# Performance work log

Hardware: AMD Instinct MI355X
Metric: run time of the kernel (lower is better)

The kernel has to match this reference:

```python
import jax, jax.numpy as jnp
import numpy as np

N, E, B = 50000, 800000, 16
IN_DIM, ED, HD, SD, NC = 64, 8, 128, 128, 8
T_STEPS = (8 + 16) // 2  # eval mode: (t_min + t_max) // 2 = 12


def setup_inputs() -> dict:
    key = jax.random.key(0)
    ks = jax.random.split(key, 12)
    s = 0.05  # small init scale so 12 residual steps stay bounded
    return {
        "x": jax.random.normal(ks[0], (N, IN_DIM), jnp.float32),
        "edge_index": jax.random.randint(ks[1], (2, E), 0, N, jnp.int64),
        "edge_attr": jax.random.normal(ks[2], (E, ED), jnp.float32),
        "batch": jnp.sort(jax.random.randint(ks[3], (N,), 0, B, jnp.int64)),
        "enc_w": jax.random.normal(ks[4], (IN_DIM, SD), jnp.float32) * s,
        "enc_b": jnp.zeros((SD,), jnp.float32),
        "msg_w": jax.random.normal(ks[5], (SD + ED, HD), jnp.float32) * s,
        "msg_b": jnp.zeros((HD,), jnp.float32),
        "up_w1": jax.random.normal(ks[6], (SD + HD, HD), jnp.float32) * s,
        "up_b1": jnp.zeros((HD,), jnp.float32),
        "up_w2": jax.random.normal(ks[7], (HD, SD), jnp.float32) * s,
        "up_b2": jnp.zeros((SD,), jnp.float32),
    }


def reference(x, edge_index, edge_attr, batch, enc_w, enc_b, msg_w, msg_b,
              up_w1, up_b1, up_w2, up_b2):
    src, dst = edge_index[0], edge_index[1]  # x_j = x[src], aggregate at dst
    # in-degree for mean aggregation (zero-degree nodes get 0, clamp avoids /0)
    deg = jax.ops.segment_sum(jnp.ones((E,), x.dtype), dst, num_segments=N)
    deg = jnp.clip(deg, 1.0)[:, None]

    # Encoder: Linear + ReLU
    state = jax.nn.relu(x @ enc_w + enc_b)  # [N, SD]

    for _ in range(T_STEPS):
        # message: relu(W_msg @ [h_j || e_ji])
        m = jax.nn.relu(jnp.concatenate([state[src], edge_attr], axis=-1) @ msg_w + msg_b)  # [E, HD]
        agg = jax.ops.segment_sum(m, dst, num_segments=N) / deg  # scatter-mean [N, HD]
        # update MLP on [h_i || m_bar_i]
        h = jax.nn.relu(jnp.concatenate([state, agg], axis=-1) @ up_w1 + up_b1)
        delta = h @ up_w2 + up_b2
        state = state + delta  # eval: no stochastic mask, no noise

    # Readout: per-graph mean over class channels
    class_ch = state[:, -NC:]  # [N, NC]
    cnt = jax.ops.segment_sum(jnp.ones((N,), x.dtype), batch, num_segments=B)
    logits = jax.ops.segment_sum(class_ch, batch, num_segments=B) / jnp.clip(cnt, 1.0)[:, None]
    return logits
```

## Files before the change

### kernel.cpp

```cpp
#include <hip/hip_runtime.h>
#include <hip/hip_bf16.h>

#define NN 50000
#define NE 800000
#define NB 16
#define T_STEPS 12
#define SCAN_B 196
#define EAW_BLOCKS 1024

typedef __attribute__((ext_vector_type(8))) short short8;
typedef __attribute__((ext_vector_type(4))) float f32x4;
typedef __attribute__((ext_vector_type(2))) float f32x2;
typedef unsigned short u16;
typedef unsigned int u32;

__device__ __forceinline__ float bf2f(u32 u) {
    union { u32 i; float f; } v; v.i = u << 16; return v.f;
}
__device__ __forceinline__ u16 f2bf(float f) {
    union { float f; u32 i; } v; v.f = f;
    u32 r = v.i + 0x7fffu + ((v.i >> 16) & 1u);
    return (u16)(r >> 16);
}
__device__ __forceinline__ f32x4 mfma16(short8 a, short8 b, f32x4 c) {
    return __builtin_amdgcn_mfma_f32_16x16x32_bf16(a, b, c, 0, 0, 0);
}

__device__ __forceinline__ u32 pk2_fp8(float o0, float o1) {
#if __has_builtin(__builtin_amdgcn_cvt_pk_fp8_f32)
    return (u32)__builtin_amdgcn_cvt_pk_fp8_f32(o0, o1, 0, false);
#else
    u32 a = 0;
    asm("v_cvt_pk_fp8_f32 %0, %1, %2" : "+v"(a) : "v"(o0), "v"(o1));
    return a;
#endif
}
__device__ __forceinline__ u32 pk4_fp8(float o0, float o1, float o2, float o3) {
    return (pk2_fp8(o0, o1) & 0xffffu) | (pk2_fp8(o2, o3) << 16);
}

__device__ __forceinline__ void fp8x4f(u32 w, float& f0, float& f1, float& f2, float& f3) {
#if __has_builtin(__builtin_amdgcn_cvt_pk_f32_fp8)
    f32x2 r0 = __builtin_amdgcn_cvt_pk_f32_fp8((int)w, false);
    f32x2 r1 = __builtin_amdgcn_cvt_pk_f32_fp8((int)w, true);
    f0 = r0[0]; f1 = r0[1]; f2 = r1[0]; f3 = r1[1];
#else
    f32x2 r0, r1;
    u32 hi = w >> 16;
    asm("v_cvt_pk_f32_fp8 %0, %1" : "=v"(r0) : "v"(w));
    asm("v_cvt_pk_f32_fp8 %0, %1" : "=v"(r1) : "v"(hi));
    f0 = r0[0]; f1 = r0[1]; f2 = r1[0]; f3 = r1[1];
#endif
}

#define W1OFF 0
#define W2OFF 32768
#define WSOFF 49152
#define ENCOFF 65536
#define PACKN 73728


__global__ void k_hist(const int* __restrict__ dst, int* __restrict__ hist) {
    int e = blockIdx.x * 256 + threadIdx.x;
    if (e < NE) atomicAdd(&hist[dst[e]], 1);
}

__global__ void k_scanA(const int* __restrict__ hist, int* __restrict__ excl,
                        int* __restrict__ bsum) {
    __shared__ int sh[256];
    int t = threadIdx.x, b = blockIdx.x;
    int idx = b * 256 + t;
    int v = (idx < NN) ? hist[idx] : 0;
    sh[t] = v;
    __syncthreads();
    for (int off = 1; off < 256; off <<= 1) {
        int add = (t >= off) ? sh[t - off] : 0;
        __syncthreads();
        sh[t] += add;
        __syncthreads();
    }
    if (idx < NN) excl[idx] = sh[t] - v;
    if (t == 255) bsum[b] = sh[255];
}

__global__ void k_scanB(int* __restrict__ bsum) {
    __shared__ int sh[256];
    int t = threadIdx.x;
    int v = (t < SCAN_B) ? bsum[t] : 0;
    sh[t] = v;
    __syncthreads();
    for (int off = 1; off < 256; off <<= 1) {
        int add = (t >= off) ? sh[t - off] : 0;
        __syncthreads();
        sh[t] += add;
        __syncthreads();
    }
    if (t < SCAN_B) bsum[t] = sh[t] - v;
}

__global__ void k_scanC(const int* __restrict__ excl, const int* __restrict__ bsum,
                        int* __restrict__ rowptr, int* __restrict__ cursor) {
    int idx = blockIdx.x * 256 + threadIdx.x;
    if (idx < NN) {
        int r = excl[idx] + bsum[blockIdx.x];
        rowptr[idx] = r;
        cursor[idx] = r;
    }
    if (idx == 0) rowptr[NN] = NE;
}

__global__ void k_scatter(const int* __restrict__ src, const int* __restrict__ dst,
                          const float* __restrict__ eattr, int* __restrict__ cursor,
                          int* __restrict__ ssrc, u16* __restrict__ ea8) {
    int e = blockIdx.x * 256 + threadIdx.x;
    if (e >= NE) return;
    int d = dst[e];
    int pos = atomicAdd(&cursor[d], 1);
    ssrc[pos] = src[e];
    const float* ap = eattr + (size_t)e * 8;
    uint4 w;
    w.x = (u32)f2bf(ap[0]) | ((u32)f2bf(ap[1]) << 16);
    w.y = (u32)f2bf(ap[2]) | ((u32)f2bf(ap[3]) << 16);
    w.z = (u32)f2bf(ap[4]) | ((u32)f2bf(ap[5]) << 16);
    w.w = (u32)f2bf(ap[6]) | ((u32)f2bf(ap[7]) << 16);
    *(uint4*)(ea8 + (size_t)pos * 8) = w;
}

__global__ __launch_bounds__(256) void k_eaw(
    const u16* __restrict__ ea8, const float* __restrict__ msg_w,
    unsigned char* __restrict__ eaw) {
    const int tid = threadIdx.x;
    const int oct = tid & 7;
    const int esub = tid >> 3;
    float w[8][16];
#pragma unroll
    for (int k = 0; k < 8; ++k) {
#pragma unroll
        for (int c4 = 0; c4 < 4; ++c4) {
            float4 v = *(const float4*)(msg_w + (size_t)(128 + k) * 128 + oct * 16 + c4 * 4);
            w[k][c4 * 4 + 0] = v.x; w[k][c4 * 4 + 1] = v.y;
            w[k][c4 * 4 + 2] = v.z; w[k][c4 * 4 + 3] = v.w;
        }
    }
    int e = blockIdx.x * 32 + esub;
    if (e >= NE) return;
    uint4 ev = *(const uint4*)(ea8 + (size_t)e * 8);
    while (true) {
        int en = e + EAW_BLOCKS * 32;
        bool more = en < NE;
        uint4 evn;
        if (more) evn = *(const uint4*)(ea8 + (size_t)en * 8);
        float ef[8];
        ef[0] = bf2f(ev.x & 0xffffu); ef[1] = bf2f(ev.x >> 16);
        ef[2] = bf2f(ev.y & 0xffffu); ef[3] = bf2f(ev.y >> 16);
        ef[4] = bf2f(ev.z & 0xffffu); ef[5] = bf2f(ev.z >> 16);
        ef[6] = bf2f(ev.w & 0xffffu); ef[7] = bf2f(ev.w >> 16);
        float o[16];
#pragma unroll
        for (int c = 0; c < 16; ++c) o[c] = ef[0] * w[0][c];
#pragma unroll
        for (int k = 1; k < 8; ++k)
#pragma unroll
            for (int c = 0; c < 16; ++c) o[c] += ef[k] * w[k][c];
        uint4 q;
        q.x = pk4_fp8(o[0], o[1], o[2], o[3]);
        q.y = pk4_fp8(o[4], o[5], o[6], o[7]);
        q.z = pk4_fp8(o[8], o[9], o[10], o[11]);
        q.w = pk4_fp8(o[12], o[13], o[14], o[15]);
        *(uint4*)(eaw + (size_t)e * 128 + oct * 16) = q;
        if (!more) break;
        ev = evn;
        e = en;
    }
}

__global__ void k_pack(const float* __restrict__ up_w1, const float* __restrict__ up_w2,
                       const float* __restrict__ msg_w, const float* __restrict__ enc_w,
                       u16* __restrict__ packed) {
    int idx = blockIdx.x * 256 + threadIdx.x;
    if (idx >= PACKN) return;
    const float* srcp; int local;
    if (idx < W2OFF)        { srcp = up_w1; local = idx; }
    else if (idx < WSOFF)   { srcp = up_w2; local = idx - W2OFF; }
    else if (idx < ENCOFF)  { srcp = msg_w; local = idx - WSOFF; }
    else                    { srcp = enc_w; local = idx - ENCOFF; }
    int j = local & 7;
    int l = (local >> 3) & 63;
    int ntks = local >> 9;
    int nt = ntks & 7;
    int ks = ntks >> 3;
    int krow = ks * 32 + (l >> 4) * 8 + j;
    int col = nt * 16 + (l & 15);
    packed[idx] = f2bf(srcp[krow * 128 + col]);
}


__global__ __launch_bounds__(256) void k_encode(
    const float* __restrict__ x, const float* __restrict__ enc_b,
    const float* __restrict__ msg_b, const u16* __restrict__ packed,
    float* __restrict__ state_f, u16* __restrict__ state_h, u16* __restrict__ swb) {
    __shared__ u16 stage[4][2048];
    const int wv = threadIdx.x >> 6, l = threadIdx.x & 63;
    const int lr = l & 15, kb = l >> 4;
    const int rb = blockIdx.x * 64 + wv * 16;
    const int row = rb + lr;
    const int rowc = row < NN ? row : NN - 1;

    f32x4 acc[8] = {};
#pragma unroll
    for (int ks = 0; ks < 2; ++ks) {
        const float* ap = x + (size_t)rowc * 64 + ks * 32 + kb * 8;
        float4 a0 = *(const float4*)ap;
        float4 a1 = *(const float4*)(ap + 4);
        short8 a;
        a[0] = (short)f2bf(a0.x); a[1] = (short)f2bf(a0.y);
        a[2] = (short)f2bf(a0.z); a[3] = (short)f2bf(a0.w);
        a[4] = (short)f2bf(a1.x); a[5] = (short)f2bf(a1.y);
        a[6] = (short)f2bf(a1.z); a[7] = (short)f2bf(a1.w);
        const u16* bp = packed + ENCOFF + (size_t)(ks * 512 + l) * 8;
#pragma unroll
        for (int nt = 0; nt < 8; ++nt) {
            short8 b = *(const short8*)(bp + nt * 512);
            acc[nt] = mfma16(a, b, acc[nt]);
        }
    }
#pragma unroll
    for (int nt = 0; nt < 8; ++nt) {
        int col = nt * 16 + lr;
        float bias = enc_b[col];
#pragma unroll
        for (int j = 0; j < 4; ++j) {
            int rl = kb * 4 + j;
            int r = rb + rl;
            float v = acc[nt][j] + bias;
            v = v > 0.f ? v : 0.f;
            u16 h = f2bf(v);
            if (r < NN) {
                state_f[(size_t)r * 128 + col] = v;
                state_h[(size_t)r * 128 + col] = h;
            }
            int byte = (rl * 256 + col * 2) ^ ((rl & 7) << 4);
            *(u16*)((char*)stage[wv] + byte) = h;
        }
    }
    f32x4 acc3[8] = {};
#pragma unroll
    for (int ks = 0; ks < 4; ++ks) {
        int byte = (lr * 256 + ks * 64 + kb * 16) ^ ((lr & 7) << 4);
        short8 a = *(const short8*)((char*)stage[wv] + byte);
        const u16* bp = packed + WSOFF + (size_t)(ks * 512 + l) * 8;
#pragma unroll
        for (int nt = 0; nt < 8; ++nt) {
            short8 b = *(const short8*)(bp + nt * 512);
            acc3[nt] = mfma16(a, b, acc3[nt]);
        }
    }
#pragma unroll
    for (int nt = 0; nt < 8; ++nt) {
        int col = nt * 16 + lr;
        float bias = msg_b[col];
#pragma unroll
        for (int j = 0; j < 4; ++j) {
            int r = rb + kb * 4 + j;
            if (r < NN) swb[(size_t)r * 128 + col] = f2bf(acc3[nt][j] + bias);
        }
    }
}


__global__ __launch_bounds__(256) void k_edge(
    const int* __restrict__ rowptr, const int* __restrict__ ssrc,
    const unsigned char* __restrict__ eaw, const u16* __restrict__ swb,
    u16* __restrict__ aggb) {
    const int wv = threadIdx.x >> 6, l = threadIdx.x & 63;
    const int half = l >> 5, lo = l & 31;
    const int n = blockIdx.x * 8 + wv * 2 + half;
    if (n >= NN) return;
    const int e0 = rowptr[n], e1 = rowptr[n + 1];
    const unsigned char* ep = eaw + (size_t)e0 * 128 + 4 * lo;
    const u16* swbase = swb + 4 * lo;
    float a0 = 0.f, a1 = 0.f, a2 = 0.f, a3 = 0.f;
#pragma unroll 4
    for (int i = e0; i < e1; ++i) {
        int s = ssrc[i];
        u32 q = *(const u32*)ep;
        ep += 128;
        uint2 swp = *(const uint2*)(swbase + (size_t)s * 128);
        float ex0, ex1, ex2, ex3;
        fp8x4f(q, ex0, ex1, ex2, ex3);
        union { u32 i; float f; } w0, w1, w2, w3;
        w0.i = swp.x << 16;
        w1.i = swp.x & 0xffff0000u;
        w2.i = swp.y << 16;
        w3.i = swp.y & 0xffff0000u;
        float m0 = w0.f + ex0, m1 = w1.f + ex1, m2 = w2.f + ex2, m3 = w3.f + ex3;
        a0 += m0 > 0.f ? m0 : 0.f;
        a1 += m1 > 0.f ? m1 : 0.f;
        a2 += m2 > 0.f ? m2 : 0.f;
        a3 += m3 > 0.f ? m3 : 0.f;
    }
    int dg = e1 - e0;
    float inv = 1.f / (float)(dg > 0 ? dg : 1);
    uint2 outw;
    outw.x = (u32)f2bf(a0 * inv) | ((u32)f2bf(a1 * inv) << 16);
    outw.y = (u32)f2bf(a2 * inv) | ((u32)f2bf(a3 * inv) << 16);
    *(uint2*)(aggb + (size_t)n * 128 + 4 * lo) = outw;
}


__global__ __launch_bounds__(256) void k_update(
    const float* __restrict__ up_b1, const float* __restrict__ up_b2,
    const float* __restrict__ msg_b, const u16* __restrict__ packed,
    const u16* __restrict__ aggb, float* __restrict__ state_f,
    u16* __restrict__ state_h, u16* __restrict__ swb) {
    __shared__ u16 stage[4][2][2048];
    const int wv = threadIdx.x >> 6, l = threadIdx.x & 63;
    const int lr = l & 15, kb = l >> 4;
    const int rbase = blockIdx.x * 128 + wv * 32;

    f32x4 acc[2][8] = {};
#pragma unroll
    for (int ks = 0; ks < 8; ++ks) {
        short8 a[2];
#pragma unroll
        for (int rt = 0; rt < 2; ++rt) {
            int row = rbase + rt * 16 + lr;
            int rowc = row < NN ? row : NN - 1;
            const u16* abase = (ks < 4)
                ? (state_h + (size_t)rowc * 128 + ks * 32 + kb * 8)
                : (aggb + (size_t)rowc * 128 + (ks - 4) * 32 + kb * 8);
            a[rt] = *(const short8*)abase;
        }
        const u16* bp = packed + W1OFF + (size_t)(ks * 512 + l) * 8;
#pragma unroll
        for (int nt = 0; nt < 8; ++nt) {
            short8 b = *(const short8*)(bp + nt * 512);
            acc[0][nt] = mfma16(a[0], b, acc[0][nt]);
            acc[1][nt] = mfma16(a[1], b, acc[1][nt]);
        }
    }
#pragma unroll
    for (int nt = 0; nt < 8; ++nt) {
        int col = nt * 16 + lr;
        float b1v = up_b1[col];
#pragma unroll
        for (int rt = 0; rt < 2; ++rt) {
#pragma unroll
            for (int j = 0; j < 4; ++j) {
                int rl = kb * 4 + j;
                float v = acc[rt][nt][j] + b1v;
                v = v > 0.f ? v : 0.f;
                int byte = (rl * 256 + col * 2) ^ ((rl & 7) << 4);
                *(u16*)((char*)stage[wv][rt] + byte) = f2bf(v);
            }
        }
    }
    f32x4 acc2[2][8] = {};
#pragma unroll
    for (int ks = 0; ks < 4; ++ks) {
        int byte = (lr * 256 + ks * 64 + kb * 16) ^ ((lr & 7) << 4);
        short8 a[2];
        a[0] = *(const short8*)((char*)stage[wv][0] + byte);
        a[1] = *(const short8*)((char*)stage[wv][1] + byte);
        const u16* bp = packed + W2OFF + (size_t)(ks * 512 + l) * 8;
#pragma unroll
        for (int nt = 0; nt < 8; ++nt) {
            short8 b = *(const short8*)(bp + nt * 512);
            acc2[0][nt] = mfma16(a[0], b, acc2[0][nt]);
            acc2[1][nt] = mfma16(a[1], b, acc2[1][nt]);
        }
    }
#pragma unroll
    for (int rt = 0; rt < 2; ++rt) {
#pragma unroll
        for (int nt = 0; nt < 8; ++nt) {
            int col = nt * 16 + lr;
            float b2v = up_b2[col];
#pragma unroll
            for (int j = 0; j < 4; ++j) {
                int rl = kb * 4 + j;
                int r = rbase + rt * 16 + rl;
                int rc = r < NN ? r : NN - 1;
                float snew = state_f[(size_t)rc * 128 + col] + acc2[rt][nt][j] + b2v;
                u16 hb = f2bf(snew);
                if (r < NN) {
                    state_f[(size_t)r * 128 + col] = snew;
                    state_h[(size_t)r * 128 + col] = hb;
                }
                int byte = (rl * 256 + col * 2) ^ ((rl & 7) << 4);
                *(u16*)((char*)stage[wv][rt] + byte) = hb;
            }
        }
    }
    f32x4 acc3[2][8] = {};
#pragma unroll
    for (int ks = 0; ks < 4; ++ks) {
        int byte = (lr * 256 + ks * 64 + kb * 16) ^ ((lr & 7) << 4);
        short8 a[2];
        a[0] = *(const short8*)((char*)stage[wv][0] + byte);
        a[1] = *(const short8*)((char*)stage[wv][1] + byte);
        const u16* bp = packed + WSOFF + (size_t)(ks * 512 + l) * 8;
#pragma unroll
        for (int nt = 0; nt < 8; ++nt) {
            short8 b = *(const short8*)(bp + nt * 512);
            acc3[0][nt] = mfma16(a[0], b, acc3[0][nt]);
            acc3[1][nt] = mfma16(a[1], b, acc3[1][nt]);
        }
    }
#pragma unroll
    for (int rt = 0; rt < 2; ++rt) {
#pragma unroll
        for (int nt = 0; nt < 8; ++nt) {
            int col = nt * 16 + lr;
            float bias = msg_b[col];
#pragma unroll
            for (int j = 0; j < 4; ++j) {
                int r = rbase + rt * 16 + kb * 4 + j;
                if (r < NN) swb[(size_t)r * 128 + col] = f2bf(acc3[rt][nt][j] + bias);
            }
        }
    }
}


__global__ void k_logits(const float* __restrict__ state_f, const int* __restrict__ batch,
                         float* __restrict__ out) {
    __shared__ float red[256];
    int b = blockIdx.x, t = threadIdx.x;
    int ch = t & 7, sub = t >> 3;
    int lo = 0, hi = NN;
    while (lo < hi) { int m = (lo + hi) >> 1; if (batch[m] < b) lo = m + 1; else hi = m; }
    int s0 = lo;
    lo = 0; hi = NN;
    while (lo < hi) { int m = (lo + hi) >> 1; if (batch[m] < b + 1) lo = m + 1; else hi = m; }
    int s1 = lo;
    float acc = 0.f;
    for (int n = s0 + sub; n < s1; n += 32)
        acc += state_f[(size_t)n * 128 + 120 + ch];
    red[t] = acc;
    __syncthreads();
    for (int off = 16; off >= 1; off >>= 1) {
        if (sub < off) red[t] += red[t + off * 8];
        __syncthreads();
    }
    if (sub == 0) {
        int c = s1 - s0;
        float cnt = (float)(c > 0 ? c : 1);
        out[b * 8 + ch] = red[ch] / cnt;
    }
}


extern "C" void kernel_launch(void* const* d_in, const int* in_sizes, int n_in,
                              void* d_out, int out_size, void* d_ws, size_t ws_size,
                              hipStream_t stream) {
    (void)in_sizes; (void)n_in;
    const float* x      = (const float*)d_in[0];
    const int*   eidx   = (const int*)d_in[1];
    const float* eattr  = (const float*)d_in[2];
    const int*   batch  = (const int*)d_in[3];
    const float* enc_w  = (const float*)d_in[4];
    const float* enc_b  = (const float*)d_in[5];
    const float* msg_w  = (const float*)d_in[6];
    const float* msg_b  = (const float*)d_in[7];
    const float* up_w1  = (const float*)d_in[8];
    const float* up_b1  = (const float*)d_in[9];
    const float* up_w2  = (const float*)d_in[10];
    const float* up_b2  = (const float*)d_in[11];
    const int* esrc = eidx;
    const int* edst = eidx + NE;

    char* p = (char*)d_ws;
    size_t off = 0;
    auto carve = [&](size_t bytes) -> char* {
        char* r = p + off;
        off += (bytes + 255) & ~(size_t)255;
        return r;
    };
    float* state_f = (float*)carve((size_t)NN * 128 * 4);
    u16* state_h   = (u16*)carve((size_t)NN * 128 * 2);
    u16* aggb      = (u16*)carve((size_t)NN * 128 * 2);
    u16* swb       = (u16*)carve((size_t)NN * 128 * 2);
    int* ssrc      = (int*)carve((size_t)NE * 4);
    u16* ea8       = (u16*)carve((size_t)NE * 8 * 2);
    unsigned char* eaw = (unsigned char*)carve((size_t)NE * 128);
    int* rowptr    = (int*)carve((size_t)(NN + 1) * 4);
    int* cursor    = (int*)carve((size_t)NN * 4);
    int* hist      = (int*)carve((size_t)NN * 4);
    int* sexcl     = (int*)carve((size_t)NN * 4);
    int* bsum      = (int*)carve((size_t)256 * 4);
    u16* packed    = (u16*)carve((size_t)PACKN * 2);
    if (off > ws_size) {
        hipMemsetAsync(d_out, 0xFF, (size_t)out_size * 4, stream);
        return;
    }

    hipMemsetAsync(hist, 0, (size_t)NN * 4, stream);
    k_hist<<<(NE + 255) / 256, 256, 0, stream>>>(edst, hist);
    k_scanA<<<SCAN_B, 256, 0, stream>>>(hist, sexcl, bsum);
    k_scanB<<<1, 256, 0, stream>>>(bsum);
    k_scanC<<<SCAN_B, 256, 0, stream>>>(sexcl, bsum, rowptr, cursor);
    k_scatter<<<(NE + 255) / 256, 256, 0, stream>>>(esrc, edst, eattr, cursor, ssrc, ea8);
    k_eaw<<<EAW_BLOCKS, 256, 0, stream>>>(ea8, msg_w, eaw);
    k_pack<<<(PACKN + 255) / 256, 256, 0, stream>>>(up_w1, up_w2, msg_w, enc_w, packed);
    k_encode<<<(NN + 63) / 64, 256, 0, stream>>>(x, enc_b, msg_b, packed, state_f, state_h, swb);
    for (int t = 0; t < T_STEPS; ++t) {
        k_edge<<<(NN + 7) / 8, 256, 0, stream>>>(rowptr, ssrc, eaw, swb, aggb);
        k_update<<<(NN + 127) / 128, 256, 0, stream>>>(up_b1, up_b2, msg_b, packed, aggb,
                                                       state_f, state_h, swb);
    }
    k_logits<<<NB, 256, 0, stream>>>(state_f, batch, (float*)d_out);
}
```

Measured before the change: 1.217 ms.

## Gather edge attrs by sorted edge id in eaw and batch src indices via shuffles

The scatter kernel now records the original edge id per sorted position instead of writing bf16-packed edge attributes, and the edge-weight precompute gathers fp32 edge_attr directly through that permutation. Its threads now cover 8 output channels each with twice as many blocks. The per-iteration edge kernel loads up to 32 source indices at once per half-wave and broadcasts them with shuffles, so the index load leaves the dependent gather chain. This trades the bf16 staging buffer for random fp32 reads, and the shuffle loop adds per-chunk overhead for low-degree nodes.

```diff
diff --git a/kernel.cpp b/kernel.cpp
--- a/kernel.cpp
+++ b/kernel.cpp
@@ -6,7 +6,7 @@
 #define NB 16
 #define T_STEPS 12
 #define SCAN_B 196
-#define EAW_BLOCKS 1024
+#define EAW_BLOCKS 2048
 
 typedef __attribute__((ext_vector_type(8))) short short8;
 typedef __attribute__((ext_vector_type(4))) float f32x4;
@@ -110,67 +110,55 @@
 }
 
 __global__ void k_scatter(const int* __restrict__ src, const int* __restrict__ dst,
-                          const float* __restrict__ eattr, int* __restrict__ cursor,
-                          int* __restrict__ ssrc, u16* __restrict__ ea8) {
+                          int* __restrict__ cursor, int* __restrict__ ssrc,
+                          int* __restrict__ seid) {
     int e = blockIdx.x * 256 + threadIdx.x;
     if (e >= NE) return;
     int d = dst[e];
     int pos = atomicAdd(&cursor[d], 1);
     ssrc[pos] = src[e];
-    const float* ap = eattr + (size_t)e * 8;
-    uint4 w;
-    w.x = (u32)f2bf(ap[0]) | ((u32)f2bf(ap[1]) << 16);
-    w.y = (u32)f2bf(ap[2]) | ((u32)f2bf(ap[3]) << 16);
-    w.z = (u32)f2bf(ap[4]) | ((u32)f2bf(ap[5]) << 16);
-    w.w = (u32)f2bf(ap[6]) | ((u32)f2bf(ap[7]) << 16);
-    *(uint4*)(ea8 + (size_t)pos * 8) = w;
+    seid[pos] = e;
 }
 
 __global__ __launch_bounds__(256) void k_eaw(
-    const u16* __restrict__ ea8, const float* __restrict__ msg_w,
-    unsigned char* __restrict__ eaw) {
+    const int* __restrict__ seid, const float* __restrict__ eattr,
+    const float* __restrict__ msg_w, unsigned char* __restrict__ eaw) {
     const int tid = threadIdx.x;
-    const int oct = tid & 7;
-    const int esub = tid >> 3;
-    float w[8][16];
+    const int hex = tid & 15;
+    const int esub = tid >> 4;
+    float w[8][8];
 #pragma unroll
     for (int k = 0; k < 8; ++k) {
-#pragma unroll
-        for (int c4 = 0; c4 < 4; ++c4) {
-            float4 v = *(const float4*)(msg_w + (size_t)(128 + k) * 128 + oct * 16 + c4 * 4);
-            w[k][c4 * 4 + 0] = v.x; w[k][c4 * 4 + 1] = v.y;
-            w[k][c4 * 4 + 2] = v.z; w[k][c4 * 4 + 3] = v.w;
-        }
-    }
-    int e = blockIdx.x * 32 + esub;
-    if (e >= NE) return;
-    uint4 ev = *(const uint4*)(ea8 + (size_t)e * 8);
+        float4 v0 = *(const float4*)(msg_w + (size_t)(128 + k) * 128 + hex * 8);
+        float4 v1 = *(const float4*)(msg_w + (size_t)(128 + k) * 128 + hex * 8 + 4);
+        w[k][0] = v0.x; w[k][1] = v0.y; w[k][2] = v0.z; w[k][3] = v0.w;
+        w[k][4] = v1.x; w[k][5] = v1.y; w[k][6] = v1.z; w[k][7] = v1.w;
+    }
+    int p = blockIdx.x * 16 + esub;
+    if (p >= NE) return;
+    int eid = seid[p];
     while (true) {
-        int en = e + EAW_BLOCKS * 32;
-        bool more = en < NE;
-        uint4 evn;
-        if (more) evn = *(const uint4*)(ea8 + (size_t)en * 8);
-        float ef[8];
-        ef[0] = bf2f(ev.x & 0xffffu); ef[1] = bf2f(ev.x >> 16);
-        ef[2] = bf2f(ev.y & 0xffffu); ef[3] = bf2f(ev.y >> 16);
-        ef[4] = bf2f(ev.z & 0xffffu); ef[5] = bf2f(ev.z >> 16);
-        ef[6] = bf2f(ev.w & 0xffffu); ef[7] = bf2f(ev.w >> 16);
-        float o[16];
-#pragma unroll
-        for (int c = 0; c < 16; ++c) o[c] = ef[0] * w[0][c];
+        int pn = p + EAW_BLOCKS * 16;
+        bool more = pn < NE;
+        int eidn = more ? seid[pn] : 0;
+        const float* ar = eattr + (size_t)eid * 8;
+        float4 a0 = *(const float4*)ar;
+        float4 a1 = *(const float4*)(ar + 4);
+        float ef[8] = {a0.x, a0.y, a0.z, a0.w, a1.x, a1.y, a1.z, a1.w};
+        float o[8];
+#pragma unroll
+        for (int c = 0; c < 8; ++c) o[c] = ef[0] * w[0][c];
 #pragma unroll
         for (int k = 1; k < 8; ++k)
 #pragma unroll
-            for (int c = 0; c < 16; ++c) o[c] += ef[k] * w[k][c];
-        uint4 q;
+            for (int c = 0; c < 8; ++c) o[c] += ef[k] * w[k][c];
+        uint2 q;
         q.x = pk4_fp8(o[0], o[1], o[2], o[3]);
         q.y = pk4_fp8(o[4], o[5], o[6], o[7]);
-        q.z = pk4_fp8(o[8], o[9], o[10], o[11]);
-        q.w = pk4_fp8(o[12], o[13], o[14], o[15]);
-        *(uint4*)(eaw + (size_t)e * 128 + oct * 16) = q;
+        *(uint2*)(eaw + (size_t)p * 128 + hex * 8) = q;
         if (!more) break;
-        ev = evn;
-        e = en;
+        p = pn;
+        eid = eidn;
     }
 }
 
@@ -277,27 +265,31 @@
     const int n = blockIdx.x * 8 + wv * 2 + half;
     if (n >= NN) return;
     const int e0 = rowptr[n], e1 = rowptr[n + 1];
-    const unsigned char* ep = eaw + (size_t)e0 * 128 + 4 * lo;
     const u16* swbase = swb + 4 * lo;
     float a0 = 0.f, a1 = 0.f, a2 = 0.f, a3 = 0.f;
+    for (int base = e0; base < e1; base += 32) {
+        int rem = e1 - base;
+        int cnt = rem > 32 ? 32 : rem;
+        int sv = ssrc[base + (lo < cnt ? lo : cnt - 1)];
+        const unsigned char* ebase = eaw + (size_t)base * 128 + 4 * lo;
 #pragma unroll 4
-    for (int i = e0; i < e1; ++i) {
-        int s = ssrc[i];
-        u32 q = *(const u32*)ep;
-        ep += 128;
-        uint2 swp = *(const uint2*)(swbase + (size_t)s * 128);
-        float ex0, ex1, ex2, ex3;
-        fp8x4f(q, ex0, ex1, ex2, ex3);
-        union { u32 i; float f; } w0, w1, w2, w3;
-        w0.i = swp.x << 16;
-        w1.i = swp.x & 0xffff0000u;
-        w2.i = swp.y << 16;
-        w3.i = swp.y & 0xffff0000u;
-        float m0 = w0.f + ex0, m1 = w1.f + ex1, m2 = w2.f + ex2, m3 = w3.f + ex3;
-        a0 += m0 > 0.f ? m0 : 0.f;
-        a1 += m1 > 0.f ? m1 : 0.f;
-        a2 += m2 > 0.f ? m2 : 0.f;
-        a3 += m3 > 0.f ? m3 : 0.f;
+        for (int j = 0; j < cnt; ++j) {
+            int s = __shfl(sv, half * 32 + j);
+            u32 q = *(const u32*)(ebase + (size_t)j * 128);
+            uint2 swp = *(const uint2*)(swbase + (size_t)s * 128);
+            float ex0, ex1, ex2, ex3;
+            fp8x4f(q, ex0, ex1, ex2, ex3);
+            union { u32 i; float f; } w0, w1, w2, w3;
+            w0.i = swp.x << 16;
+            w1.i = swp.x & 0xffff0000u;
+            w2.i = swp.y << 16;
+            w3.i = swp.y & 0xffff0000u;
+            float m0 = w0.f + ex0, m1 = w1.f + ex1, m2 = w2.f + ex2, m3 = w3.f + ex3;
+            a0 += m0 > 0.f ? m0 : 0.f;
+            a1 += m1 > 0.f ? m1 : 0.f;
+            a2 += m2 > 0.f ? m2 : 0.f;
+            a3 += m3 > 0.f ? m3 : 0.f;
+        }
     }
     int dg = e1 - e0;
     float inv = 1.f / (float)(dg > 0 ? dg : 1);
@@ -482,7 +474,7 @@
     u16* aggb      = (u16*)carve((size_t)NN * 128 * 2);
     u16* swb       = (u16*)carve((size_t)NN * 128 * 2);
     int* ssrc      = (int*)carve((size_t)NE * 4);
-    u16* ea8       = (u16*)carve((size_t)NE * 8 * 2);
+    int* seid      = (int*)carve((size_t)NE * 4);
     unsigned char* eaw = (unsigned char*)carve((size_t)NE * 128);
     int* rowptr    = (int*)carve((size_t)(NN + 1) * 4);
     int* cursor    = (int*)carve((size_t)NN * 4);
@@ -500,8 +492,8 @@
     k_scanA<<<SCAN_B, 256, 0, stream>>>(hist, sexcl, bsum);
     k_scanB<<<1, 256, 0, stream>>>(bsum);
     k_scanC<<<SCAN_B, 256, 0, stream>>>(sexcl, bsum, rowptr, cursor);
-    k_scatter<<<(NE + 255) / 256, 256, 0, stream>>>(esrc, edst, eattr, cursor, ssrc, ea8);
-    k_eaw<<<EAW_BLOCKS, 256, 0, stream>>>(ea8, msg_w, eaw);
+    k_scatter<<<(NE + 255) / 256, 256, 0, stream>>>(esrc, edst, cursor, ssrc, seid);
+    k_eaw<<<EAW_BLOCKS, 256, 0, stream>>>(seid, eattr, msg_w, eaw);
     k_pack<<<(PACKN + 255) / 256, 256, 0, stream>>>(up_w1, up_w2, msg_w, enc_w, packed);
     k_encode<<<(NN + 63) / 64, 256, 0, stream>>>(x, enc_b, msg_b, packed, state_f, state_h, swb);
     for (int t = 0; t < T_STEPS; ++t) {
```

After: 1.286 ms. 5.6% more time.
